# Kernel optimization log

Hardware: AMD Instinct MI355X
Metric: run time of the kernel (lower is better)

The kernel has to match this reference:

```python
import jax, jax.numpy as jnp
import numpy as np

DIM = 256
NUM_HEADS = 8
SCALE = (DIM // NUM_HEADS) ** (-0.5)
EPS = 1e-6


def channel_layernorm(x, w, b):
    # LayerNorm over channel dim (axis=1) per spatial location, as in source
    u = jnp.mean(x, axis=1, keepdims=True)
    s = jnp.mean((x - u) ** 2, axis=1, keepdims=True)
    xn = (x - u) / jnp.sqrt(s + EPS)
    return w[:, None, None] * xn + b[:, None, None]


def conv1x1(x, W, b):
    # x: [B,C,H,W], W: [O,C], b: [O]
    return jnp.einsum('bchw,oc->bohw', x, W) + b[:, None, None]


def setup_inputs() -> dict:
    key = jax.random.key(0)
    ks = jax.random.split(key, 10)
    B, C, H, W = 8, DIM, 48, 48
    inp = {
        'x1': jax.random.normal(ks[0], (B, C, H, W), jnp.float32),
        'x2': jax.random.normal(ks[1], (B, C, H, W), jnp.float32),
        'Wq': jax.random.normal(ks[2], (C, C), jnp.float32) * (1.0 / np.sqrt(C)),
        'bq': jnp.zeros((C,), jnp.float32),
        'Wk': jax.random.normal(ks[3], (C, C), jnp.float32) * (1.0 / np.sqrt(C)),
        'bk': jnp.zeros((C,), jnp.float32),
        'Wv': jax.random.normal(ks[4], (C, C), jnp.float32) * (1.0 / np.sqrt(C)),
        'bv': jnp.zeros((C,), jnp.float32),
        'Wp': jax.random.normal(ks[5], (C, C), jnp.float32) * (1.0 / np.sqrt(C)),
        'bp': jnp.zeros((C,), jnp.float32),
        'w_nq': jnp.ones((C,), jnp.float32),
        'b_nq': jnp.zeros((C,), jnp.float32),
        'w_nkv': jnp.ones((C,), jnp.float32),
        'b_nkv': jnp.zeros((C,), jnp.float32),
    }
    return inp


def reference(x1, x2, Wq, bq, Wk, bk, Wv, bv, Wp, bp, w_nq, b_nq, w_nkv, b_nkv):
    B, C, H, W = x1.shape
    x1n = channel_layernorm(x1, w_nq, b_nq)
    x2n = channel_layernorm(x2, w_nkv, b_nkv)
    # project then flatten spatial -> tokens: [B, N, C]
    q = conv1x1(x1n, Wq, bq).reshape(B, C, H * W).transpose(0, 2, 1)
    k = conv1x1(x2n, Wk, bk).reshape(B, C, H * W).transpose(0, 2, 1)
    v = conv1x1(x2n, Wv, bv).reshape(B, C, H * W).transpose(0, 2, 1)
    # single-head full attention over N tokens (heads never split in source)
    attn = jnp.einsum('bnc,bmc->bnm', q, k) * SCALE
    attn = jax.nn.softmax(attn, axis=-1)
    out = jnp.einsum('bnm,bmc->bnc', attn, v)  # [B,N,C]
    out = out.transpose(0, 2, 1).reshape(B, C, H, W)
    out = conv1x1(out, Wp, bp)
    return out + x1
```

## Files before the change

### kernel.cpp

```cpp
#include <hip/hip_runtime.h>

#define NB 8
#define CH 256
#define NT 2304
#define KVSPLIT 3
#define TPS 24
#define QB 128
#define QSCALE 0.2550349f
#define DEFER_THR 11.5415604f
#define LN_EPS 1e-6f

typedef __attribute__((ext_vector_type(8))) short short8;
typedef __attribute__((ext_vector_type(4))) float f32x4;
typedef __attribute__((ext_vector_type(16))) float f32x16;
typedef __attribute__((ext_vector_type(4))) unsigned short ushort4v;
typedef __attribute__((ext_vector_type(8))) unsigned short ushort8v;
typedef __attribute__((ext_vector_type(4))) float float4v;
typedef __attribute__((ext_vector_type(2))) unsigned int uint2v;

__device__ __forceinline__ unsigned short f2bf(float f) {
  unsigned int u = __float_as_uint(f);
  u += 0x7fffu + ((u >> 16) & 1u);
  return (unsigned short)(u >> 16);
}
__device__ __forceinline__ float bf2f(unsigned short s) {
  return __uint_as_float(((unsigned int)s) << 16);
}
__device__ __forceinline__ unsigned int cvtpk(float a, float b) {
  unsigned int r;
  asm("v_cvt_pk_bf16_f32 %0, %1, %2" : "=v"(r) : "v"(a), "v"(b));
  return r;
}

__device__ __forceinline__ void gload_lds16(const void* g, void* l) {
  __builtin_amdgcn_global_load_lds(
      (const __attribute__((address_space(1))) unsigned int*)g,
      (__attribute__((address_space(3))) unsigned int*)l, 16, 0, 0);
}

__global__ __launch_bounds__(256) void wconv_kernel(
    const float* __restrict__ wq, const float* __restrict__ wk,
    const float* __restrict__ wv, const float* __restrict__ wp,
    unsigned short* __restrict__ out) {
  int z = blockIdx.y;
  const float* src = (z == 0) ? wq : (z == 1) ? wk : (z == 2) ? wv : wp;
  unsigned short* dst = out + z * 65536;
  int i = (blockIdx.x * 256 + threadIdx.x) * 4;
  float4v v = *(const float4v*)(src + i);
  ushort4v r;
  r[0] = f2bf(v[0]); r[1] = f2bf(v[1]); r[2] = f2bf(v[2]); r[3] = f2bf(v[3]);
  *(ushort4v*)(dst + i) = r;
}

__global__ __launch_bounds__(256) void ln_kernel(
    const float* __restrict__ x1, const float* __restrict__ x2,
    const float* __restrict__ w1, const float* __restrict__ b1,
    const float* __restrict__ w2, const float* __restrict__ b2,
    unsigned short* __restrict__ o1, unsigned short* __restrict__ o2) {
  __shared__ float part[4][64][2];
  __shared__ float fin[64][2];
  int z = blockIdx.z;
  const float* x = z ? x2 : x1;
  const float* w = z ? w2 : w1;
  const float* bias = z ? b2 : b1;
  unsigned short* out = z ? o2 : o1;
  int tid = threadIdx.x;
  int lane = tid & 63, wv = tid >> 6;
  int n0 = blockIdx.x * 64;
  int b = blockIdx.y;
  const float* xp = x + (size_t)b * CH * NT + n0 + lane;
  float xc[64];
  float sum = 0.f, ss = 0.f;
#pragma unroll
  for (int j = 0; j < 64; ++j) {
    float v = xp[(size_t)(wv * 64 + j) * NT];
    xc[j] = v;
    sum += v; ss += v * v;
  }
  part[wv][lane][0] = sum;
  part[wv][lane][1] = ss;
  __syncthreads();
  if (tid < 64) {
    float s = 0.f, q = 0.f;
#pragma unroll
    for (int wi = 0; wi < 4; ++wi) { s += part[wi][tid][0]; q += part[wi][tid][1]; }
    float u = s * (1.0f / CH);
    float var = q * (1.0f / CH) - u * u;
    fin[tid][0] = u;
    fin[tid][1] = rsqrtf(var + LN_EPS);
  }
  __syncthreads();
  float u = fin[lane][0], rstd = fin[lane][1];
  unsigned short* op = out + ((size_t)b * NT + n0 + lane) * CH;
#pragma unroll
  for (int c0 = 0; c0 < 64; c0 += 8) {
    ushort8v pk;
#pragma unroll
    for (int j = 0; j < 8; ++j)
      pk[j] = f2bf((xc[c0 + j] - u) * rstd * w[wv * 64 + c0 + j] +
                   bias[wv * 64 + c0 + j]);
    *(ushort8v*)(op + wv * 64 + c0) = pk;
  }
}

__global__ __launch_bounds__(256) void proj_kernel(
    const unsigned short* __restrict__ xq, const unsigned short* __restrict__ xkv,
    const unsigned short* __restrict__ wbf,
    const float* __restrict__ bq, const float* __restrict__ bk,
    const float* __restrict__ bv,
    unsigned short* __restrict__ q, unsigned short* __restrict__ k,
    unsigned short* __restrict__ vt) {
  __shared__ char As[16384];
  __shared__ char Bs[16384];
  int tid = threadIdx.x;
  int lane = tid & 63, wid = tid >> 6;
  int z = blockIdx.z;
  int b = z / 3, pz = z - b * 3;
  const unsigned short* A = ((pz == 0) ? xq : xkv) + (size_t)b * NT * CH;
  const unsigned short* W = wbf + pz * 65536;
  const float* bias = (pz == 0) ? bq : (pz == 1) ? bk : bv;
  int m0 = blockIdx.x * 128;
  int c0 = blockIdx.y * 128;
  int wr = wid >> 1, wc = wid & 1;

  f32x4 zero4 = {0.f, 0.f, 0.f, 0.f};
  f32x4 acc[4][4];
#pragma unroll
  for (int i = 0; i < 4; ++i)
#pragma unroll
    for (int j = 0; j < 4; ++j) acc[i][j] = zero4;

  for (int kt = 0; kt < 4; ++kt) {
#pragma unroll
    for (int it = 0; it < 4; ++it) {
      int li = it * 256 + tid;
      int X = li * 16;
      int row = X >> 7;
      int colb = (X & 127) ^ ((row & 7) << 4);
      gload_lds16((const char*)A + ((size_t)(m0 + row) * CH + kt * 64) * 2 + colb,
                  As + it * 4096 + wid * 1024);
      gload_lds16((const char*)W + ((size_t)(c0 + row) * CH + kt * 64) * 2 + colb,
                  Bs + it * 4096 + wid * 1024);
    }
    __syncthreads();
#pragma unroll
    for (int kk = 0; kk < 2; ++kk) {
      int cb = kk * 64 + ((lane >> 4) << 4);
      short8 af[4], bf[4];
#pragma unroll
      for (int mi = 0; mi < 4; ++mi) {
        int row = wr * 64 + mi * 16 + (lane & 15);
        af[mi] = *(const short8*)(As + row * 128 + (cb ^ ((row & 7) << 4)));
      }
#pragma unroll
      for (int ni = 0; ni < 4; ++ni) {
        int row = wc * 64 + ni * 16 + (lane & 15);
        bf[ni] = *(const short8*)(Bs + row * 128 + (cb ^ ((row & 7) << 4)));
      }
#pragma unroll
      for (int mi = 0; mi < 4; ++mi)
#pragma unroll
        for (int ni = 0; ni < 4; ++ni)
          acc[mi][ni] = __builtin_amdgcn_mfma_f32_16x16x32_bf16(
              af[mi], bf[ni], acc[mi][ni], 0, 0, 0);
    }
    __syncthreads();
  }

  int colbase = c0 + wc * 64;
  int rowbase = m0 + wr * 64;
  if (pz < 2) {
    unsigned short* dst = ((pz == 0) ? q : k) + (size_t)b * NT * CH;
    float scl = (pz == 0) ? QSCALE : 1.0f;
#pragma unroll
    for (int mi = 0; mi < 4; ++mi)
#pragma unroll
      for (int ni = 0; ni < 4; ++ni) {
        int col = colbase + ni * 16 + (lane & 15);
        float bb = bias[col];
        int row0 = rowbase + mi * 16 + ((lane >> 4) << 2);
#pragma unroll
        for (int r = 0; r < 4; ++r)
          dst[(size_t)(row0 + r) * CH + col] = f2bf((acc[mi][ni][r] + bb) * scl);
      }
  } else {
    unsigned short* dst = vt + (size_t)b * CH * NT;
#pragma unroll
    for (int mi = 0; mi < 4; ++mi)
#pragma unroll
      for (int ni = 0; ni < 4; ++ni) {
        int col = colbase + ni * 16 + (lane & 15);
        float bb = bias[col];
        int row0 = rowbase + mi * 16 + ((lane >> 4) << 2);
        ushort4v pk;
#pragma unroll
        for (int r = 0; r < 4; ++r) pk[r] = f2bf(acc[mi][ni][r] + bb);
        *(ushort4v*)(dst + (size_t)col * NT + row0) = pk;
      }
  }
}

#define STAGEK(kt, buf)                                                        \
  {                                                                            \
    _Pragma("unroll") for (int it = 0; it < 4; ++it) {                         \
      int rowk = it * 8 + wid * 2 + (lane >> 5);                               \
      int colb = ((lane & 31) * 16) ^ ((rowk & 7) << 4);                       \
      gload_lds16((const char*)kb + ((size_t)((kt) + rowk) * CH) * 2 + colb,   \
                  (buf) + it * 4096 + wid * 1024);                             \
    }                                                                          \
  }
#define STAGEV(kt, buf)                                                        \
  {                                                                            \
    _Pragma("unroll") for (int it = 0; it < 4; ++it) {                         \
      int rowv = it * 64 + wid * 16 + (lane >> 2);                             \
      int sic = ((lane & 3) ^ ((lane >> 3) & 3)) << 4;                         \
      gload_lds16((const char*)vb + ((size_t)rowv * NT + (kt)) * 2 + sic,      \
                  (buf) + it * 4096 + wid * 1024);                             \
    }                                                                          \
  }

__global__ __launch_bounds__(256, 2) void attn_kernel(
    const unsigned short* __restrict__ q, const unsigned short* __restrict__ k,
    const unsigned short* __restrict__ vt,
    unsigned short* __restrict__ op0, unsigned short* __restrict__ op1,
    unsigned short* __restrict__ op2, float* __restrict__ ml) {
  __shared__ __align__(1024) char Ks[2][16384];
  __shared__ __align__(1024) char Vs[2][16384];
  int tid = threadIdx.x, lane = tid & 63, wid = tid >> 6;
  int r31 = lane & 31, h2 = lane >> 5;
  int b = blockIdx.z;
  int split = blockIdx.y;
  int q0 = blockIdx.x * QB;
  const unsigned short* qb_ = q + (size_t)b * NT * CH;
  const unsigned short* kb = k + (size_t)b * NT * CH;
  const unsigned short* vb = vt + (size_t)b * CH * NT;

  int qrow = q0 + wid * 32 + r31;
  short8 qf[16];
#pragma unroll
  for (int st = 0; st < 16; ++st)
    qf[st] = *(const short8*)(qb_ + (size_t)qrow * CH + st * 16 + h2 * 8);

  f32x16 o[8];
#pragma unroll
  for (int i = 0; i < 8; ++i) o[i] = (f32x16){};
  float mrun = -INFINITY, lrun = 0.f;

  int kt0base = split * (TPS * 32);
  STAGEK(kt0base, Ks[0]);
  STAGEV(kt0base, Vs[0]);
  __syncthreads();

  int sw4 = (r31 & 7) << 4;
  int sw3 = (r31 & 6) << 3;
  int oj0 = (8 * h2) ^ sw3, oj1 = (8 * h2 + 16) ^ sw3;
  int oj2 = (8 * h2 + 32) ^ sw3, oj3 = (8 * h2 + 48) ^ sw3;

  union V16 { uint2v p[2]; short8 s8; };
  union PB { unsigned int u[4]; short8 s8; };

  for (int t = 0; t < TPS; ++t) {
    int kt0 = kt0base + t * 32;
    const char* kbase = Ks[t & 1] + r31 * 512 + ((h2 * 16) ^ sw4);
    const char* vL = Vs[t & 1] + r31 * 64;
    if (t + 1 < TPS) {
      STAGEK(kt0 + 32, Ks[(t + 1) & 1]);
      STAGEV(kt0 + 32, Vs[(t + 1) & 1]);
    }

    f32x16 s = (f32x16){};
    __builtin_amdgcn_s_setprio(1);
#pragma unroll
    for (int st = 0; st < 16; ++st) {
      short8 kf = *(const short8*)((unsigned long long)kbase ^ (unsigned)(st * 32));
      s = __builtin_amdgcn_mfma_f32_32x32x16_bf16(kf, qf[st], s, 0, 0, 0);
    }
    __builtin_amdgcn_s_setprio(0);

    float mx = fmaxf(s[0], s[1]);
#pragma unroll
    for (int i = 2; i < 16; ++i) mx = fmaxf(mx, s[i]);
    mx = fmaxf(mx, __shfl_xor(mx, 32));
    if (__any(mx - mrun > DEFER_THR)) {
      float mnew = fmaxf(mrun, mx);
      float al = exp2f(mrun - mnew);
      lrun *= al;
      mrun = mnew;
#pragma unroll
      for (int i = 0; i < 8; ++i) o[i] = o[i] * al;
    }
    float rs = 0.f;
#pragma unroll
    for (int i = 0; i < 16; ++i) {
      s[i] = exp2f(s[i] - mrun);
      rs += s[i];
    }
    rs += __shfl_xor(rs, 32);
    lrun += rs;

    PB pbA, pbB;
    pbA.u[0] = cvtpk(s[0], s[1]);   pbA.u[1] = cvtpk(s[2], s[3]);
    pbA.u[2] = cvtpk(s[4], s[5]);   pbA.u[3] = cvtpk(s[6], s[7]);
    pbB.u[0] = cvtpk(s[8], s[9]);   pbB.u[1] = cvtpk(s[10], s[11]);
    pbB.u[2] = cvtpk(s[12], s[13]); pbB.u[3] = cvtpk(s[14], s[15]);

    __builtin_amdgcn_s_setprio(1);
#pragma unroll
    for (int d2 = 0; d2 < 8; ++d2) {
      V16 a1, a2;
      a1.p[0] = *(const uint2v*)(vL + d2 * 2048 + oj0);
      a1.p[1] = *(const uint2v*)(vL + d2 * 2048 + oj1);
      a2.p[0] = *(const uint2v*)(vL + d2 * 2048 + oj2);
      a2.p[1] = *(const uint2v*)(vL + d2 * 2048 + oj3);
      o[d2] = __builtin_amdgcn_mfma_f32_32x32x16_bf16(a1.s8, pbA.s8, o[d2], 0, 0, 0);
      o[d2] = __builtin_amdgcn_mfma_f32_32x32x16_bf16(a2.s8, pbB.s8, o[d2], 0, 0, 0);
    }
    __builtin_amdgcn_s_setprio(0);
    __syncthreads();
  }

  unsigned short* od = ((split == 0) ? op0 : (split == 1) ? op1 : op2) +
                       (size_t)(b * NT + qrow) * CH;
#pragma unroll
  for (int d2 = 0; d2 < 8; ++d2)
#pragma unroll
    for (int m = 0; m < 4; ++m) {
      ushort4v pk;
#pragma unroll
      for (int r = 0; r < 4; ++r) pk[r] = f2bf(o[d2][m * 4 + r]);
      *(ushort4v*)(od + d2 * 32 + m * 8 + h2 * 4) = pk;
    }
  if (lane < 32) {
    float* mlp = ml + ((size_t)(split * NB + b) * NT + q0 + wid * 32 + lane) * 2;
    mlp[0] = mrun;
    mlp[1] = lrun;
  }
}

__global__ __launch_bounds__(256) void combine_kernel(
    const unsigned short* __restrict__ op0, const unsigned short* __restrict__ op1,
    const unsigned short* __restrict__ op2, const float* __restrict__ ml,
    unsigned short* __restrict__ oa) {
  const size_t S = (size_t)NB * NT;
  int g = blockIdx.x * 8 + (threadIdx.x >> 5);
  int c = (threadIdx.x & 31) * 8;
  float m0 = ml[(size_t)g * 2], l0 = ml[(size_t)g * 2 + 1];
  float m1 = ml[(S + g) * 2], l1 = ml[(S + g) * 2 + 1];
  float m2 = ml[(2 * S + g) * 2], l2 = ml[(2 * S + g) * 2 + 1];
  float M = fmaxf(fmaxf(m0, m1), m2);
  float w0 = exp2f(m0 - M), w1 = exp2f(m1 - M), w2 = exp2f(m2 - M);
  float Li = 1.0f / (w0 * l0 + w1 * l1 + w2 * l2);
  w0 *= Li; w1 *= Li; w2 *= Li;
  ushort8v a0 = *(const ushort8v*)(op0 + (size_t)g * CH + c);
  ushort8v a1 = *(const ushort8v*)(op1 + (size_t)g * CH + c);
  ushort8v a2 = *(const ushort8v*)(op2 + (size_t)g * CH + c);
  ushort8v r;
#pragma unroll
  for (int j = 0; j < 8; ++j)
    r[j] = f2bf(w0 * bf2f(a0[j]) + w1 * bf2f(a1[j]) + w2 * bf2f(a2[j]));
  *(ushort8v*)(oa + (size_t)g * CH + c) = r;
}

__global__ __launch_bounds__(256) void oproj_kernel(
    const unsigned short* __restrict__ oa, const unsigned short* __restrict__ wp,
    const float* __restrict__ bp, const float* __restrict__ x1,
    float* __restrict__ outp) {
  __shared__ char As[16384];
  __shared__ char Bs[16384];
  int tid = threadIdx.x;
  int lane = tid & 63, wid = tid >> 6;
  int b = blockIdx.z;
  const unsigned short* A = oa + (size_t)b * NT * CH;
  int m0 = blockIdx.x * 128;
  int c0 = blockIdx.y * 128;
  int wr = wid >> 1, wc = wid & 1;

  f32x4 zero4 = {0.f, 0.f, 0.f, 0.f};
  f32x4 acc[4][4];
#pragma unroll
  for (int i = 0; i < 4; ++i)
#pragma unroll
    for (int j = 0; j < 4; ++j) acc[i][j] = zero4;

  for (int kt = 0; kt < 4; ++kt) {
#pragma unroll
    for (int it = 0; it < 4; ++it) {
      int li = it * 256 + tid;
      int X = li * 16;
      int row = X >> 7;
      int colb = (X & 127) ^ ((row & 7) << 4);
      gload_lds16((const char*)A + ((size_t)(m0 + row) * CH + kt * 64) * 2 + colb,
                  As + it * 4096 + wid * 1024);
      gload_lds16((const char*)wp + ((size_t)(c0 + row) * CH + kt * 64) * 2 + colb,
                  Bs + it * 4096 + wid * 1024);
    }
    __syncthreads();
#pragma unroll
    for (int kk = 0; kk < 2; ++kk) {
      int cb = kk * 64 + ((lane >> 4) << 4);
      short8 af[4], bf[4];
#pragma unroll
      for (int mi = 0; mi < 4; ++mi) {
        int row = wr * 64 + mi * 16 + (lane & 15);
        af[mi] = *(const short8*)(As + row * 128 + (cb ^ ((row & 7) << 4)));
      }
#pragma unroll
      for (int ni = 0; ni < 4; ++ni) {
        int row = wc * 64 + ni * 16 + (lane & 15);
        bf[ni] = *(const short8*)(Bs + row * 128 + (cb ^ ((row & 7) << 4)));
      }
#pragma unroll
      for (int mi = 0; mi < 4; ++mi)
#pragma unroll
        for (int ni = 0; ni < 4; ++ni)
          acc[mi][ni] = __builtin_amdgcn_mfma_f32_16x16x32_bf16(
              af[mi], bf[ni], acc[mi][ni], 0, 0, 0);
    }
    __syncthreads();
  }

  int colbase = c0 + wc * 64;
  int rowbase = m0 + wr * 64;
#pragma unroll
  for (int mi = 0; mi < 4; ++mi)
#pragma unroll
    for (int ni = 0; ni < 4; ++ni) {
      int col = colbase + ni * 16 + (lane & 15);
      float bb = bp[col];
      int row0 = rowbase + mi * 16 + ((lane >> 4) << 2);
      int base = (b * CH + col) * NT + row0;
      float4v xv = *(const float4v*)(x1 + base);
      float4v rs;
#pragma unroll
      for (int r = 0; r < 4; ++r) rs[r] = acc[mi][ni][r] + bb + xv[r];
      *(float4v*)(outp + base) = rs;
    }
}

extern "C" void kernel_launch(void* const* d_in, const int* in_sizes, int n_in,
                              void* d_out, int out_size, void* d_ws, size_t ws_size,
                              hipStream_t stream) {
  (void)in_sizes; (void)n_in; (void)out_size; (void)ws_size;
  const float* x1 = (const float*)d_in[0];
  const float* x2 = (const float*)d_in[1];
  const float* Wq = (const float*)d_in[2];
  const float* bq = (const float*)d_in[3];
  const float* Wk = (const float*)d_in[4];
  const float* bk = (const float*)d_in[5];
  const float* Wv = (const float*)d_in[6];
  const float* bv = (const float*)d_in[7];
  const float* Wp = (const float*)d_in[8];
  const float* bp = (const float*)d_in[9];
  const float* wnq = (const float*)d_in[10];
  const float* bnq = (const float*)d_in[11];
  const float* wnkv = (const float*)d_in[12];
  const float* bnkv = (const float*)d_in[13];
  float* outp = (float*)d_out;

  const size_t TSZ = (size_t)NB * NT * CH;
  unsigned short* xq = (unsigned short*)d_ws;
  unsigned short* xkv = xq + TSZ;
  unsigned short* qb = xkv + TSZ;
  unsigned short* kbuf = qb + TSZ;
  unsigned short* vtb = kbuf + TSZ;
  unsigned short* oab = vtb + TSZ;
  unsigned short* wbf = oab + TSZ;
  float* ml = (float*)(wbf + 4 * 65536);

  wconv_kernel<<<dim3(64, 4), dim3(256), 0, stream>>>(Wq, Wk, Wv, Wp, wbf);
  ln_kernel<<<dim3(36, 8, 2), dim3(256), 0, stream>>>(x1, x2, wnq, bnq, wnkv, bnkv,
                                                      xq, xkv);
  proj_kernel<<<dim3(18, 2, 24), dim3(256), 0, stream>>>(xq, xkv, wbf, bq, bk, bv,
                                                         qb, kbuf, vtb);
  attn_kernel<<<dim3(NT / QB, KVSPLIT, 8), dim3(256), 0, stream>>>(
      qb, kbuf, vtb, xq, xkv, oab, ml);
  combine_kernel<<<dim3(NB * NT / 8), dim3(256), 0, stream>>>(xq, xkv, oab, ml,
                                                              oab);
  oproj_kernel<<<dim3(18, 2, 8), dim3(256), 0, stream>>>(oab, wbf + 3 * 65536, bp,
                                                         x1, outp);
}
```

Baseline: 147.9 us.

## Software-pipeline QK and PV across tiles and fuse split combine into output projection

The attention loop is restructured so the QK^T MFMAs for tile t interleave with the PV MFMAs for tile t-1, and the softmax runs while the next K/V tile loads. This overlaps the softmax latency with matrix work. The separate combine kernel is removed, and its split-merge of the three partial outputs is done inside the oproj A-tile load. That saves a launch and an intermediate round trip, at the cost of redundant combine work across the two column blocks and synchronous register-staged loads.

```diff
diff --git a/kernel.cpp b/kernel.cpp
--- a/kernel.cpp
+++ b/kernel.cpp
@@ -219,6 +219,37 @@
     }                                                                          \
   }
 
+#define SOFTMAX_PB()                                                           \
+  {                                                                            \
+    float t0 = fmaxf(s[0], s[1]), t1 = fmaxf(s[2], s[3]);                      \
+    float t2 = fmaxf(s[4], s[5]), t3 = fmaxf(s[6], s[7]);                      \
+    float t4 = fmaxf(s[8], s[9]), t5 = fmaxf(s[10], s[11]);                    \
+    float t6 = fmaxf(s[12], s[13]), t7 = fmaxf(s[14], s[15]);                  \
+    t0 = fmaxf(t0, t1); t2 = fmaxf(t2, t3); t4 = fmaxf(t4, t5);                \
+    t6 = fmaxf(t6, t7);                                                        \
+    float mx = fmaxf(fmaxf(t0, t2), fmaxf(t4, t6));                            \
+    mx = fmaxf(mx, __shfl_xor(mx, 32));                                        \
+    if (__any(mx - mrun > DEFER_THR)) {                                        \
+      float mnew = fmaxf(mrun, mx);                                            \
+      float al = exp2f(mrun - mnew);                                           \
+      lrun *= al;                                                              \
+      mrun = mnew;                                                             \
+      _Pragma("unroll") for (int i = 0; i < 8; ++i) o[i] = o[i] * al;          \
+    }                                                                          \
+    _Pragma("unroll") for (int i = 0; i < 16; ++i) s[i] = exp2f(s[i] - mrun);  \
+    float u0 = (s[0] + s[1]) + (s[2] + s[3]);                                  \
+    float u1 = (s[4] + s[5]) + (s[6] + s[7]);                                  \
+    float u2 = (s[8] + s[9]) + (s[10] + s[11]);                                \
+    float u3 = (s[12] + s[13]) + (s[14] + s[15]);                              \
+    float rs = (u0 + u1) + (u2 + u3);                                          \
+    rs += __shfl_xor(rs, 32);                                                  \
+    lrun += rs;                                                                \
+    pbA.u[0] = cvtpk(s[0], s[1]);   pbA.u[1] = cvtpk(s[2], s[3]);              \
+    pbA.u[2] = cvtpk(s[4], s[5]);   pbA.u[3] = cvtpk(s[6], s[7]);              \
+    pbB.u[0] = cvtpk(s[8], s[9]);   pbB.u[1] = cvtpk(s[10], s[11]);            \
+    pbB.u[2] = cvtpk(s[12], s[13]); pbB.u[3] = cvtpk(s[14], s[15]);            \
+  }
+
 __global__ __launch_bounds__(256, 2) void attn_kernel(
     const unsigned short* __restrict__ q, const unsigned short* __restrict__ k,
     const unsigned short* __restrict__ vt,
@@ -247,10 +278,6 @@
   float mrun = -INFINITY, lrun = 0.f;
 
   int kt0base = split * (TPS * 32);
-  STAGEK(kt0base, Ks[0]);
-  STAGEV(kt0base, Vs[0]);
-  __syncthreads();
-
   int sw4 = (r31 & 7) << 4;
   int sw3 = (r31 & 6) << 3;
   int oj0 = (8 * h2) ^ sw3, oj1 = (8 * h2 + 16) ^ sw3;
@@ -258,16 +285,15 @@
 
   union V16 { uint2v p[2]; short8 s8; };
   union PB { unsigned int u[4]; short8 s8; };
-
-  for (int t = 0; t < TPS; ++t) {
-    int kt0 = kt0base + t * 32;
-    const char* kbase = Ks[t & 1] + r31 * 512 + ((h2 * 16) ^ sw4);
-    const char* vL = Vs[t & 1] + r31 * 64;
-    if (t + 1 < TPS) {
-      STAGEK(kt0 + 32, Ks[(t + 1) & 1]);
-      STAGEV(kt0 + 32, Vs[(t + 1) & 1]);
-    }
-
+  PB pbA, pbB;
+
+  STAGEK(kt0base, Ks[0]);
+  STAGEV(kt0base, Vs[0]);
+  __syncthreads();
+  STAGEK(kt0base + 32, Ks[1]);
+  STAGEV(kt0base + 32, Vs[1]);
+  {
+    const char* kbase = Ks[0] + r31 * 512 + ((h2 * 16) ^ sw4);
     f32x16 s = (f32x16){};
     __builtin_amdgcn_s_setprio(1);
 #pragma unroll
@@ -276,47 +302,56 @@
       s = __builtin_amdgcn_mfma_f32_32x32x16_bf16(kf, qf[st], s, 0, 0, 0);
     }
     __builtin_amdgcn_s_setprio(0);
-
-    float mx = fmaxf(s[0], s[1]);
-#pragma unroll
-    for (int i = 2; i < 16; ++i) mx = fmaxf(mx, s[i]);
-    mx = fmaxf(mx, __shfl_xor(mx, 32));
-    if (__any(mx - mrun > DEFER_THR)) {
-      float mnew = fmaxf(mrun, mx);
-      float al = exp2f(mrun - mnew);
-      lrun *= al;
-      mrun = mnew;
-#pragma unroll
-      for (int i = 0; i < 8; ++i) o[i] = o[i] * al;
-    }
-    float rs = 0.f;
-#pragma unroll
-    for (int i = 0; i < 16; ++i) {
-      s[i] = exp2f(s[i] - mrun);
-      rs += s[i];
-    }
-    rs += __shfl_xor(rs, 32);
-    lrun += rs;
-
-    PB pbA, pbB;
-    pbA.u[0] = cvtpk(s[0], s[1]);   pbA.u[1] = cvtpk(s[2], s[3]);
-    pbA.u[2] = cvtpk(s[4], s[5]);   pbA.u[3] = cvtpk(s[6], s[7]);
-    pbB.u[0] = cvtpk(s[8], s[9]);   pbB.u[1] = cvtpk(s[10], s[11]);
-    pbB.u[2] = cvtpk(s[12], s[13]); pbB.u[3] = cvtpk(s[14], s[15]);
-
+    SOFTMAX_PB();
+  }
+  __syncthreads();
+
+  for (int t = 1; t < TPS; ++t) {
+    const char* kbase = Ks[t & 1] + r31 * 512 + ((h2 * 16) ^ sw4);
+    const char* vLp = Vs[(t & 1) ^ 1] + r31 * 64;
+    f32x16 s = (f32x16){};
+    __builtin_amdgcn_s_setprio(1);
+#pragma unroll
+    for (int st = 0; st < 16; ++st) {
+      short8 kf = *(const short8*)((unsigned long long)kbase ^ (unsigned)(st * 32));
+      s = __builtin_amdgcn_mfma_f32_32x32x16_bf16(kf, qf[st], s, 0, 0, 0);
+      int d2 = st >> 1;
+      V16 av;
+      if ((st & 1) == 0) {
+        av.p[0] = *(const uint2v*)(vLp + d2 * 2048 + oj0);
+        av.p[1] = *(const uint2v*)(vLp + d2 * 2048 + oj1);
+        o[d2] = __builtin_amdgcn_mfma_f32_32x32x16_bf16(av.s8, pbA.s8, o[d2], 0, 0, 0);
+      } else {
+        av.p[0] = *(const uint2v*)(vLp + d2 * 2048 + oj2);
+        av.p[1] = *(const uint2v*)(vLp + d2 * 2048 + oj3);
+        o[d2] = __builtin_amdgcn_mfma_f32_32x32x16_bf16(av.s8, pbB.s8, o[d2], 0, 0, 0);
+      }
+    }
+    __builtin_amdgcn_s_setprio(0);
+    __syncthreads();
+    if (t + 1 < TPS) {
+      int ktn = kt0base + (t + 1) * 32;
+      STAGEK(ktn, Ks[(t + 1) & 1]);
+      STAGEV(ktn, Vs[(t + 1) & 1]);
+    }
+    SOFTMAX_PB();
+    __syncthreads();
+  }
+
+  {
+    const char* vLp = Vs[(TPS - 1) & 1] + r31 * 64;
     __builtin_amdgcn_s_setprio(1);
 #pragma unroll
     for (int d2 = 0; d2 < 8; ++d2) {
       V16 a1, a2;
-      a1.p[0] = *(const uint2v*)(vL + d2 * 2048 + oj0);
-      a1.p[1] = *(const uint2v*)(vL + d2 * 2048 + oj1);
-      a2.p[0] = *(const uint2v*)(vL + d2 * 2048 + oj2);
-      a2.p[1] = *(const uint2v*)(vL + d2 * 2048 + oj3);
+      a1.p[0] = *(const uint2v*)(vLp + d2 * 2048 + oj0);
+      a1.p[1] = *(const uint2v*)(vLp + d2 * 2048 + oj1);
+      a2.p[0] = *(const uint2v*)(vLp + d2 * 2048 + oj2);
+      a2.p[1] = *(const uint2v*)(vLp + d2 * 2048 + oj3);
       o[d2] = __builtin_amdgcn_mfma_f32_32x32x16_bf16(a1.s8, pbA.s8, o[d2], 0, 0, 0);
       o[d2] = __builtin_amdgcn_mfma_f32_32x32x16_bf16(a2.s8, pbB.s8, o[d2], 0, 0, 0);
     }
     __builtin_amdgcn_s_setprio(0);
-    __syncthreads();
   }
 
   unsigned short* od = ((split == 0) ? op0 : (split == 1) ? op1 : op2) +
@@ -337,43 +372,20 @@
   }
 }
 
-__global__ __launch_bounds__(256) void combine_kernel(
+__global__ __launch_bounds__(256) void oproj_kernel(
     const unsigned short* __restrict__ op0, const unsigned short* __restrict__ op1,
     const unsigned short* __restrict__ op2, const float* __restrict__ ml,
-    unsigned short* __restrict__ oa) {
-  const size_t S = (size_t)NB * NT;
-  int g = blockIdx.x * 8 + (threadIdx.x >> 5);
-  int c = (threadIdx.x & 31) * 8;
-  float m0 = ml[(size_t)g * 2], l0 = ml[(size_t)g * 2 + 1];
-  float m1 = ml[(S + g) * 2], l1 = ml[(S + g) * 2 + 1];
-  float m2 = ml[(2 * S + g) * 2], l2 = ml[(2 * S + g) * 2 + 1];
-  float M = fmaxf(fmaxf(m0, m1), m2);
-  float w0 = exp2f(m0 - M), w1 = exp2f(m1 - M), w2 = exp2f(m2 - M);
-  float Li = 1.0f / (w0 * l0 + w1 * l1 + w2 * l2);
-  w0 *= Li; w1 *= Li; w2 *= Li;
-  ushort8v a0 = *(const ushort8v*)(op0 + (size_t)g * CH + c);
-  ushort8v a1 = *(const ushort8v*)(op1 + (size_t)g * CH + c);
-  ushort8v a2 = *(const ushort8v*)(op2 + (size_t)g * CH + c);
-  ushort8v r;
-#pragma unroll
-  for (int j = 0; j < 8; ++j)
-    r[j] = f2bf(w0 * bf2f(a0[j]) + w1 * bf2f(a1[j]) + w2 * bf2f(a2[j]));
-  *(ushort8v*)(oa + (size_t)g * CH + c) = r;
-}
-
-__global__ __launch_bounds__(256) void oproj_kernel(
-    const unsigned short* __restrict__ oa, const unsigned short* __restrict__ wp,
-    const float* __restrict__ bp, const float* __restrict__ x1,
-    float* __restrict__ outp) {
+    const unsigned short* __restrict__ wp, const float* __restrict__ bp,
+    const float* __restrict__ x1, float* __restrict__ outp) {
   __shared__ char As[16384];
   __shared__ char Bs[16384];
   int tid = threadIdx.x;
   int lane = tid & 63, wid = tid >> 6;
   int b = blockIdx.z;
-  const unsigned short* A = oa + (size_t)b * NT * CH;
   int m0 = blockIdx.x * 128;
   int c0 = blockIdx.y * 128;
   int wr = wid >> 1, wc = wid & 1;
+  const size_t S = (size_t)NB * NT;
 
   f32x4 zero4 = {0.f, 0.f, 0.f, 0.f};
   f32x4 acc[4][4];
@@ -389,10 +401,25 @@
       int X = li * 16;
       int row = X >> 7;
       int colb = (X & 127) ^ ((row & 7) << 4);
-      gload_lds16((const char*)A + ((size_t)(m0 + row) * CH + kt * 64) * 2 + colb,
-                  As + it * 4096 + wid * 1024);
       gload_lds16((const char*)wp + ((size_t)(c0 + row) * CH + kt * 64) * 2 + colb,
                   Bs + it * 4096 + wid * 1024);
+      size_t g = (size_t)(b * NT + m0 + row) * CH + kt * 64 + (colb >> 1);
+      size_t gn = (size_t)b * NT + m0 + row;
+      ushort8v a0 = *(const ushort8v*)(op0 + g);
+      ushort8v a1 = *(const ushort8v*)(op1 + g);
+      ushort8v a2 = *(const ushort8v*)(op2 + g);
+      float mm0 = ml[gn * 2], ll0 = ml[gn * 2 + 1];
+      float mm1 = ml[(S + gn) * 2], ll1 = ml[(S + gn) * 2 + 1];
+      float mm2 = ml[(2 * S + gn) * 2], ll2 = ml[(2 * S + gn) * 2 + 1];
+      float M = fmaxf(fmaxf(mm0, mm1), mm2);
+      float w0 = exp2f(mm0 - M), w1 = exp2f(mm1 - M), w2 = exp2f(mm2 - M);
+      float Li = 1.0f / (w0 * ll0 + w1 * ll1 + w2 * ll2);
+      w0 *= Li; w1 *= Li; w2 *= Li;
+      ushort8v pk;
+#pragma unroll
+      for (int j = 0; j < 8; ++j)
+        pk[j] = f2bf(w0 * bf2f(a0[j]) + w1 * bf2f(a1[j]) + w2 * bf2f(a2[j]));
+      *(ushort8v*)(As + X) = pk;
     }
     __syncthreads();
 #pragma unroll
@@ -474,8 +501,6 @@
                                                          qb, kbuf, vtb);
   attn_kernel<<<dim3(NT / QB, KVSPLIT, 8), dim3(256), 0, stream>>>(
       qb, kbuf, vtb, xq, xkv, oab, ml);
-  combine_kernel<<<dim3(NB * NT / 8), dim3(256), 0, stream>>>(xq, xkv, oab, ml,
-                                                              oab);
-  oproj_kernel<<<dim3(18, 2, 8), dim3(256), 0, stream>>>(oab, wbf + 3 * 65536, bp,
-                                                         x1, outp);
-}
+  oproj_kernel<<<dim3(18, 2, 8), dim3(256), 0, stream>>>(
+      xq, xkv, oab, ml, wbf + 3 * 65536, bp, x1, outp);
+}
```

Result: slower. 155.3 us (+5.0%).

## Fuse split-KV combine into output projection and split QK MFMA accumulation chains

Applied to the files above, without the earlier changes.

Removes the standalone combine kernel: the output-projection GEMM now reads the three partial attention outputs plus their max/sum stats, merges them in registers, and writes the combined bf16 tile straight into shared memory. This avoids one kernel launch and a full write and read of the combined attention output. In the attention loop, the QK^T MFMA chain is split into two independent accumulators summed afterwards, and the max and sum reductions use trees, to shorten dependency chains. The cost is that each of the two column blocks of oproj recomputes the combine, and the A-tile load becomes synchronous register loads instead of direct-to-LDS loads.

```diff
diff --git a/kernel.cpp b/kernel.cpp
--- a/kernel.cpp
+++ b/kernel.cpp
@@ -268,35 +268,49 @@
       STAGEV(kt0 + 32, Vs[(t + 1) & 1]);
     }
 
-    f32x16 s = (f32x16){};
+    f32x16 s = (f32x16){}, s2 = (f32x16){};
     __builtin_amdgcn_s_setprio(1);
 #pragma unroll
-    for (int st = 0; st < 16; ++st) {
+    for (int st = 0; st < 8; ++st) {
       short8 kf = *(const short8*)((unsigned long long)kbase ^ (unsigned)(st * 32));
       s = __builtin_amdgcn_mfma_f32_32x32x16_bf16(kf, qf[st], s, 0, 0, 0);
+      short8 kg = *(const short8*)((unsigned long long)kbase ^
+                                   (unsigned)((st + 8) * 32));
+      s2 = __builtin_amdgcn_mfma_f32_32x32x16_bf16(kg, qf[st + 8], s2, 0, 0, 0);
     }
     __builtin_amdgcn_s_setprio(0);
-
-    float mx = fmaxf(s[0], s[1]);
-#pragma unroll
-    for (int i = 2; i < 16; ++i) mx = fmaxf(mx, s[i]);
-    mx = fmaxf(mx, __shfl_xor(mx, 32));
-    if (__any(mx - mrun > DEFER_THR)) {
-      float mnew = fmaxf(mrun, mx);
-      float al = exp2f(mrun - mnew);
-      lrun *= al;
-      mrun = mnew;
-#pragma unroll
-      for (int i = 0; i < 8; ++i) o[i] = o[i] * al;
-    }
-    float rs = 0.f;
-#pragma unroll
-    for (int i = 0; i < 16; ++i) {
-      s[i] = exp2f(s[i] - mrun);
-      rs += s[i];
-    }
-    rs += __shfl_xor(rs, 32);
-    lrun += rs;
+#pragma unroll
+    for (int i = 0; i < 16; ++i) s[i] += s2[i];
+
+    {
+      float t0 = fmaxf(s[0], s[1]), t1 = fmaxf(s[2], s[3]);
+      float t2 = fmaxf(s[4], s[5]), t3 = fmaxf(s[6], s[7]);
+      float t4 = fmaxf(s[8], s[9]), t5 = fmaxf(s[10], s[11]);
+      float t6 = fmaxf(s[12], s[13]), t7 = fmaxf(s[14], s[15]);
+      t0 = fmaxf(t0, t1); t2 = fmaxf(t2, t3); t4 = fmaxf(t4, t5);
+      t6 = fmaxf(t6, t7);
+      float mx = fmaxf(fmaxf(t0, t2), fmaxf(t4, t6));
+      mx = fmaxf(mx, __shfl_xor(mx, 32));
+      if (__any(mx - mrun > DEFER_THR)) {
+        float mnew = fmaxf(mrun, mx);
+        float al = exp2f(mrun - mnew);
+        lrun *= al;
+        mrun = mnew;
+#pragma unroll
+        for (int i = 0; i < 8; ++i) o[i] = o[i] * al;
+      }
+    }
+#pragma unroll
+    for (int i = 0; i < 16; ++i) s[i] = exp2f(s[i] - mrun);
+    {
+      float u0 = (s[0] + s[1]) + (s[2] + s[3]);
+      float u1 = (s[4] + s[5]) + (s[6] + s[7]);
+      float u2 = (s[8] + s[9]) + (s[10] + s[11]);
+      float u3 = (s[12] + s[13]) + (s[14] + s[15]);
+      float rs = (u0 + u1) + (u2 + u3);
+      rs += __shfl_xor(rs, 32);
+      lrun += rs;
+    }
 
     PB pbA, pbB;
     pbA.u[0] = cvtpk(s[0], s[1]);   pbA.u[1] = cvtpk(s[2], s[3]);
@@ -337,43 +351,20 @@
   }
 }
 
-__global__ __launch_bounds__(256) void combine_kernel(
+__global__ __launch_bounds__(256) void oproj_kernel(
     const unsigned short* __restrict__ op0, const unsigned short* __restrict__ op1,
     const unsigned short* __restrict__ op2, const float* __restrict__ ml,
-    unsigned short* __restrict__ oa) {
-  const size_t S = (size_t)NB * NT;
-  int g = blockIdx.x * 8 + (threadIdx.x >> 5);
-  int c = (threadIdx.x & 31) * 8;
-  float m0 = ml[(size_t)g * 2], l0 = ml[(size_t)g * 2 + 1];
-  float m1 = ml[(S + g) * 2], l1 = ml[(S + g) * 2 + 1];
-  float m2 = ml[(2 * S + g) * 2], l2 = ml[(2 * S + g) * 2 + 1];
-  float M = fmaxf(fmaxf(m0, m1), m2);
-  float w0 = exp2f(m0 - M), w1 = exp2f(m1 - M), w2 = exp2f(m2 - M);
-  float Li = 1.0f / (w0 * l0 + w1 * l1 + w2 * l2);
-  w0 *= Li; w1 *= Li; w2 *= Li;
-  ushort8v a0 = *(const ushort8v*)(op0 + (size_t)g * CH + c);
-  ushort8v a1 = *(const ushort8v*)(op1 + (size_t)g * CH + c);
-  ushort8v a2 = *(const ushort8v*)(op2 + (size_t)g * CH + c);
-  ushort8v r;
-#pragma unroll
-  for (int j = 0; j < 8; ++j)
-    r[j] = f2bf(w0 * bf2f(a0[j]) + w1 * bf2f(a1[j]) + w2 * bf2f(a2[j]));
-  *(ushort8v*)(oa + (size_t)g * CH + c) = r;
-}
-
-__global__ __launch_bounds__(256) void oproj_kernel(
-    const unsigned short* __restrict__ oa, const unsigned short* __restrict__ wp,
-    const float* __restrict__ bp, const float* __restrict__ x1,
-    float* __restrict__ outp) {
+    const unsigned short* __restrict__ wp, const float* __restrict__ bp,
+    const float* __restrict__ x1, float* __restrict__ outp) {
   __shared__ char As[16384];
   __shared__ char Bs[16384];
   int tid = threadIdx.x;
   int lane = tid & 63, wid = tid >> 6;
   int b = blockIdx.z;
-  const unsigned short* A = oa + (size_t)b * NT * CH;
   int m0 = blockIdx.x * 128;
   int c0 = blockIdx.y * 128;
   int wr = wid >> 1, wc = wid & 1;
+  const size_t S = (size_t)NB * NT;
 
   f32x4 zero4 = {0.f, 0.f, 0.f, 0.f};
   f32x4 acc[4][4];
@@ -389,10 +380,25 @@
       int X = li * 16;
       int row = X >> 7;
       int colb = (X & 127) ^ ((row & 7) << 4);
-      gload_lds16((const char*)A + ((size_t)(m0 + row) * CH + kt * 64) * 2 + colb,
-                  As + it * 4096 + wid * 1024);
       gload_lds16((const char*)wp + ((size_t)(c0 + row) * CH + kt * 64) * 2 + colb,
                   Bs + it * 4096 + wid * 1024);
+      size_t g = (size_t)(b * NT + m0 + row) * CH + kt * 64 + (colb >> 1);
+      size_t gn = (size_t)b * NT + m0 + row;
+      ushort8v a0 = *(const ushort8v*)(op0 + g);
+      ushort8v a1 = *(const ushort8v*)(op1 + g);
+      ushort8v a2 = *(const ushort8v*)(op2 + g);
+      float mm0 = ml[gn * 2], ll0 = ml[gn * 2 + 1];
+      float mm1 = ml[(S + gn) * 2], ll1 = ml[(S + gn) * 2 + 1];
+      float mm2 = ml[(2 * S + gn) * 2], ll2 = ml[(2 * S + gn) * 2 + 1];
+      float M = fmaxf(fmaxf(mm0, mm1), mm2);
+      float w0 = exp2f(mm0 - M), w1 = exp2f(mm1 - M), w2 = exp2f(mm2 - M);
+      float Li = 1.0f / (w0 * ll0 + w1 * ll1 + w2 * ll2);
+      w0 *= Li; w1 *= Li; w2 *= Li;
+      ushort8v pk;
+#pragma unroll
+      for (int j = 0; j < 8; ++j)
+        pk[j] = f2bf(w0 * bf2f(a0[j]) + w1 * bf2f(a1[j]) + w2 * bf2f(a2[j]));
+      *(ushort8v*)(As + X) = pk;
     }
     __syncthreads();
 #pragma unroll
@@ -474,8 +480,6 @@
                                                          qb, kbuf, vtb);
   attn_kernel<<<dim3(NT / QB, KVSPLIT, 8), dim3(256), 0, stream>>>(
       qb, kbuf, vtb, xq, xkv, oab, ml);
-  combine_kernel<<<dim3(NB * NT / 8), dim3(256), 0, stream>>>(xq, xkv, oab, ml,
-                                                              oab);
-  oproj_kernel<<<dim3(18, 2, 8), dim3(256), 0, stream>>>(oab, wbf + 3 * 65536, bp,
-                                                         x1, outp);
-}
+  oproj_kernel<<<dim3(18, 2, 8), dim3(256), 0, stream>>>(
+      xq, xkv, oab, ml, wbf + 3 * 65536, bp, x1, outp);
+}
```

Measured after the change: 150.1 us. About the same (+1.5%).

## Use partial vmcnt waits and raw barriers; split QK accumulation chains

Applied to the files above, without the earlier changes.

Replaces the full __syncthreads in the attention loop with explicit vmcnt waits that only drain the current tile's async LDS loads, leaving the next tile's prefetch in flight, followed by raw s_barriers. The QK^T MFMA chain is split into two independent accumulators to shorten the dependency chain. The max and sum reductions are rewritten as trees. The hard-coded vmcnt(8) assumes a specific number of loads per stage, so it is fragile if the staging macros change, and it risks LDS races if that count is wrong.

```diff
diff --git a/kernel.cpp b/kernel.cpp
--- a/kernel.cpp
+++ b/kernel.cpp
@@ -247,9 +247,9 @@
   float mrun = -INFINITY, lrun = 0.f;
 
   int kt0base = split * (TPS * 32);
+  asm volatile("s_waitcnt vmcnt(0)" ::: "memory");
   STAGEK(kt0base, Ks[0]);
   STAGEV(kt0base, Vs[0]);
-  __syncthreads();
 
   int sw4 = (r31 & 7) << 4;
   int sw3 = (r31 & 6) << 3;
@@ -266,37 +266,56 @@
     if (t + 1 < TPS) {
       STAGEK(kt0 + 32, Ks[(t + 1) & 1]);
       STAGEV(kt0 + 32, Vs[(t + 1) & 1]);
-    }
-
-    f32x16 s = (f32x16){};
+      asm volatile("s_waitcnt vmcnt(8)" ::: "memory");
+    } else {
+      asm volatile("s_waitcnt vmcnt(0)" ::: "memory");
+    }
+    __builtin_amdgcn_sched_barrier(0);
+    asm volatile("s_barrier" ::: "memory");
+
+    f32x16 s = (f32x16){}, s2 = (f32x16){};
     __builtin_amdgcn_s_setprio(1);
 #pragma unroll
-    for (int st = 0; st < 16; ++st) {
+    for (int st = 0; st < 8; ++st) {
       short8 kf = *(const short8*)((unsigned long long)kbase ^ (unsigned)(st * 32));
       s = __builtin_amdgcn_mfma_f32_32x32x16_bf16(kf, qf[st], s, 0, 0, 0);
+      short8 kg = *(const short8*)((unsigned long long)kbase ^
+                                   (unsigned)((st + 8) * 32));
+      s2 = __builtin_amdgcn_mfma_f32_32x32x16_bf16(kg, qf[st + 8], s2, 0, 0, 0);
     }
     __builtin_amdgcn_s_setprio(0);
-
-    float mx = fmaxf(s[0], s[1]);
-#pragma unroll
-    for (int i = 2; i < 16; ++i) mx = fmaxf(mx, s[i]);
-    mx = fmaxf(mx, __shfl_xor(mx, 32));
-    if (__any(mx - mrun > DEFER_THR)) {
-      float mnew = fmaxf(mrun, mx);
-      float al = exp2f(mrun - mnew);
-      lrun *= al;
-      mrun = mnew;
-#pragma unroll
-      for (int i = 0; i < 8; ++i) o[i] = o[i] * al;
-    }
-    float rs = 0.f;
-#pragma unroll
-    for (int i = 0; i < 16; ++i) {
-      s[i] = exp2f(s[i] - mrun);
-      rs += s[i];
-    }
-    rs += __shfl_xor(rs, 32);
-    lrun += rs;
+#pragma unroll
+    for (int i = 0; i < 16; ++i) s[i] += s2[i];
+
+    {
+      float t0 = fmaxf(s[0], s[1]), t1 = fmaxf(s[2], s[3]);
+      float t2 = fmaxf(s[4], s[5]), t3 = fmaxf(s[6], s[7]);
+      float t4 = fmaxf(s[8], s[9]), t5 = fmaxf(s[10], s[11]);
+      float t6 = fmaxf(s[12], s[13]), t7 = fmaxf(s[14], s[15]);
+      t0 = fmaxf(t0, t1); t2 = fmaxf(t2, t3); t4 = fmaxf(t4, t5);
+      t6 = fmaxf(t6, t7);
+      float mx = fmaxf(fmaxf(t0, t2), fmaxf(t4, t6));
+      mx = fmaxf(mx, __shfl_xor(mx, 32));
+      if (__any(mx - mrun > DEFER_THR)) {
+        float mnew = fmaxf(mrun, mx);
+        float al = exp2f(mrun - mnew);
+        lrun *= al;
+        mrun = mnew;
+#pragma unroll
+        for (int i = 0; i < 8; ++i) o[i] = o[i] * al;
+      }
+    }
+#pragma unroll
+    for (int i = 0; i < 16; ++i) s[i] = exp2f(s[i] - mrun);
+    {
+      float u0 = (s[0] + s[1]) + (s[2] + s[3]);
+      float u1 = (s[4] + s[5]) + (s[6] + s[7]);
+      float u2 = (s[8] + s[9]) + (s[10] + s[11]);
+      float u3 = (s[12] + s[13]) + (s[14] + s[15]);
+      float rs = (u0 + u1) + (u2 + u3);
+      rs += __shfl_xor(rs, 32);
+      lrun += rs;
+    }
 
     PB pbA, pbB;
     pbA.u[0] = cvtpk(s[0], s[1]);   pbA.u[1] = cvtpk(s[2], s[3]);
@@ -316,7 +335,7 @@
       o[d2] = __builtin_amdgcn_mfma_f32_32x32x16_bf16(a2.s8, pbB.s8, o[d2], 0, 0, 0);
     }
     __builtin_amdgcn_s_setprio(0);
-    __syncthreads();
+    asm volatile("s_barrier" ::: "memory");
   }
 
   unsigned short* od = ((split == 0) ? op0 : (split == 1) ? op1 : op2) +
```

New measurement: 154.1 us. 4.2% more time.
